# Performance work log

Measured on AMD Instinct MI355X. Metric: run time of the kernel, lower is better.

Reference implementation:

```python
import jax, jax.numpy as jnp
import numpy as np

NUM_EDGE_TYPES = 38
NUM_NODE_TYPES = 4
HIDDEN = 64
HOPS = 4
N_NODES = 100_000
N_EDGES = 1_600_000


def setup_inputs() -> dict:
    key = jax.random.key(0)
    ks = jax.random.split(key, 7)
    in_dim = NUM_EDGE_TYPES + 2 * NUM_NODE_TYPES  # 46
    return {
        "edge_index": jax.random.randint(ks[0], (2, N_EDGES), 0, N_NODES),
        "edge_type": jax.random.randint(ks[1], (N_EDGES,), 0, NUM_EDGE_TYPES),
        "node_type": jax.random.randint(ks[2], (N_NODES,), 0, NUM_NODE_TYPES),
        "W1": jax.random.normal(ks[3], (in_dim, HIDDEN), dtype=jnp.float32) * 0.1,
        "b1": jax.random.normal(ks[4], (HIDDEN,), dtype=jnp.float32) * 0.1,
        "W2": jax.random.normal(ks[5], (HIDDEN, 1), dtype=jnp.float32) * 0.1,
        "b2": jax.random.normal(ks[6], (1,), dtype=jnp.float32) * 0.1,
    }


def reference(edge_index, edge_type, node_type, W1, b1, W2, b2):
    src, dst = edge_index[0], edge_index[1]  # PyG: x_j = x[edge_index[0]], aggregate at edge_index[1]
    head_type = node_type[src]
    tail_type = node_type[dst]
    # Linear over concat of three one-hots == sum of three gathered weight rows + bias.
    h = (W1[edge_type]
         + W1[NUM_EDGE_TYPES + head_type]
         + W1[NUM_EDGE_TYPES + NUM_NODE_TYPES + tail_type]
         + b1)                                   # [E, HIDDEN]
    h = jax.nn.gelu(h)
    edge_emb = jax.nn.sigmoid(h @ W2 + b2)       # [E, 1]

    num_nodes = node_type.shape[0]
    aggr = jnp.zeros((num_nodes, 1), dtype=edge_emb.dtype)
    for _ in range(HOPS):
        msg = aggr[src] + edge_emb               # gather + add, [E, 1]
        aggr = jax.ops.segment_sum(msg, dst, num_segments=num_nodes)  # scatter-add
    return aggr
```

## Files before the change

### kernel.cpp

```cpp
#include <hip/hip_runtime.h>

#define NUM_EDGE_TYPES 38
#define NUM_NODE_TYPES 4
#define HIDDEN 64
#define TABLE_SIZE (NUM_EDGE_TYPES * NUM_NODE_TYPES * NUM_NODE_TYPES)
#define SRC_BITS 17
#define SRC_MASK ((1 << SRC_BITS) - 1)
#define BSHIFT 8
#define BNODES 256
#define MAXB 512
#define PB 512
#define EPT 16
#define CHUNK (PB * EPT)
#define HB 1024
#define CAPC 6144

__device__ __forceinline__ float table_entry(int i, const float* __restrict__ W1,
                                             const float* __restrict__ b1,
                                             const float* __restrict__ W2,
                                             const float* __restrict__ b2) {
    int et = i >> 4, ht = (i >> 2) & 3, tt = i & 3;
    const float* r0 = W1 + et * HIDDEN;
    const float* r1 = W1 + (NUM_EDGE_TYPES + ht) * HIDDEN;
    const float* r2 = W1 + (NUM_EDGE_TYPES + NUM_NODE_TYPES + tt) * HIDDEN;
    float acc = b2[0];
#pragma unroll 8
    for (int k = 0; k < HIDDEN; ++k) {
        float h = r0[k] + r1[k] + r2[k] + b1[k];
        float u = 0.7978845608028654f * (h + 0.044715f * h * h * h);
        float g = 0.5f * h * (1.0f + tanhf(u));
        acc += g * W2[k];
    }
    return 1.0f / (1.0f + expf(-acc));
}

__global__ void table_kernel(const float* __restrict__ W1, const float* __restrict__ b1,
                             const float* __restrict__ W2, const float* __restrict__ b2,
                             float* __restrict__ table) {
    int i = blockIdx.x * blockDim.x + threadIdx.x;
    if (i < TABLE_SIZE) table[i] = table_entry(i, W1, b1, W2, b2);
}

__global__ __launch_bounds__(PB)
void partition_kernel(const int* __restrict__ src, const int* __restrict__ dst,
                      const int* __restrict__ etype, int* __restrict__ cursor,
                      int* __restrict__ pack, int E, int nbk, int cap,
                      const float* __restrict__ W1, const float* __restrict__ b1,
                      const float* __restrict__ W2, const float* __restrict__ b2,
                      float* __restrict__ table) {
    __shared__ int hist[MAXB];
    __shared__ int locCur[MAXB];
    for (int i = threadIdx.x; i < nbk; i += PB) hist[i] = 0;
    __syncthreads();
    int start = blockIdx.x * CHUNK;
    int end = min(start + CHUNK, E);
    if (end - start == CHUNK) {
        int4 dv[4], sv[4], ev[4];
#pragma unroll
        for (int g = 0; g < 4; ++g) {
            int j = start + g * (PB * 4) + threadIdx.x * 4;
            dv[g] = *(const int4*)(dst + j);
        }
#pragma unroll
        for (int g = 0; g < 4; ++g) {
            atomicAdd(&hist[dv[g].x >> BSHIFT], 1);
            atomicAdd(&hist[dv[g].y >> BSHIFT], 1);
            atomicAdd(&hist[dv[g].z >> BSHIFT], 1);
            atomicAdd(&hist[dv[g].w >> BSHIFT], 1);
        }
#pragma unroll
        for (int g = 0; g < 4; ++g) {
            int j = start + g * (PB * 4) + threadIdx.x * 4;
            sv[g] = *(const int4*)(src + j);
            ev[g] = *(const int4*)(etype + j);
        }
        __syncthreads();
        for (int i = threadIdx.x; i < nbk; i += PB) {
            int h = hist[i];
            locCur[i] = h ? i * cap + atomicAdd(&cursor[i], h) : 0;
        }
        __syncthreads();
#pragma unroll
        for (int g = 0; g < 4; ++g) {
            int t0 = atomicAdd(&locCur[dv[g].x >> BSHIFT], 1);
            int t1 = atomicAdd(&locCur[dv[g].y >> BSHIFT], 1);
            int t2 = atomicAdd(&locCur[dv[g].z >> BSHIFT], 1);
            int t3 = atomicAdd(&locCur[dv[g].w >> BSHIFT], 1);
            pack[t0] = (ev[g].x << (SRC_BITS + 8)) | ((dv[g].x & (BNODES - 1)) << SRC_BITS) | sv[g].x;
            pack[t1] = (ev[g].y << (SRC_BITS + 8)) | ((dv[g].y & (BNODES - 1)) << SRC_BITS) | sv[g].y;
            pack[t2] = (ev[g].z << (SRC_BITS + 8)) | ((dv[g].z & (BNODES - 1)) << SRC_BITS) | sv[g].z;
            pack[t3] = (ev[g].w << (SRC_BITS + 8)) | ((dv[g].w & (BNODES - 1)) << SRC_BITS) | sv[g].w;
        }
    } else {
        for (int j = start + threadIdx.x; j < end; j += PB)
            atomicAdd(&hist[dst[j] >> BSHIFT], 1);
        __syncthreads();
        for (int i = threadIdx.x; i < nbk; i += PB) {
            int h = hist[i];
            locCur[i] = h ? i * cap + atomicAdd(&cursor[i], h) : 0;
        }
        __syncthreads();
        for (int j = start + threadIdx.x; j < end; j += PB) {
            int d = dst[j];
            int slot = atomicAdd(&locCur[d >> BSHIFT], 1);
            pack[slot] = (etype[j] << (SRC_BITS + 8)) | ((d & (BNODES - 1)) << SRC_BITS) | src[j];
        }
    }

    for (int seg = blockIdx.x; seg < 8; seg += gridDim.x) {
        int wid = threadIdx.x >> 6, lane = threadIdx.x & 63;
        int e0 = seg * 76;
        int e1 = min(e0 + 76, TABLE_SIZE);
        for (int e = e0 + wid; e < e1; e += PB / 64) {
            int et = e >> 4, ht = (e >> 2) & 3, tt = e & 3;
            float h = W1[et * HIDDEN + lane]
                    + W1[(NUM_EDGE_TYPES + ht) * HIDDEN + lane]
                    + W1[(NUM_EDGE_TYPES + NUM_NODE_TYPES + tt) * HIDDEN + lane]
                    + b1[lane];
            float u = 0.7978845608028654f * (h + 0.044715f * h * h * h);
            float g = 0.5f * h * (1.0f + tanhf(u));
            float v = g * W2[lane];
            v += __shfl_xor(v, 32, 64);
            v += __shfl_xor(v, 16, 64);
            v += __shfl_xor(v, 8, 64);
            v += __shfl_xor(v, 4, 64);
            v += __shfl_xor(v, 2, 64);
            v += __shfl_xor(v, 1, 64);
            if (lane == 0) table[e] = 1.0f / (1.0f + expf(-(v + b2[0])));
        }
    }
}

__global__ void sort_base_kernel(int* __restrict__ pack, const int* __restrict__ cursor,
                                 const int* __restrict__ ntype, const float* __restrict__ table,
                                 float* __restrict__ base, int* __restrict__ nodeOffG,
                                 int N, int cap) {
    __shared__ int rawL[CAPC];
    __shared__ int sortedL[CAPC];
    __shared__ float tbl[TABLE_SIZE];
    __shared__ int nodeCnt[BNODES];
    __shared__ int nodeOff[BNODES + 1];
    __shared__ unsigned char ntLoc[BNODES];
    int b = blockIdx.x;
    int node0 = b << BSHIFT;
    int tid = threadIdx.x;
    int st = b * cap;
    int c = min(cursor[b], cap);

    if (tid < TABLE_SIZE) tbl[tid] = table[tid];
    if (tid < BNODES) {
        nodeCnt[tid] = 0;
        int n = node0 + tid;
        ntLoc[tid] = (n < N) ? (unsigned char)ntype[n] : 0;
    }
    __syncthreads();

    int c4 = c & ~3;
    for (int j = tid * 4; j < c4; j += HB * 4) {
        int4 v = *(const int4*)(pack + st + j);
        *(int4*)(rawL + j) = v;
        atomicAdd(&nodeCnt[(v.x >> SRC_BITS) & (BNODES - 1)], 1);
        atomicAdd(&nodeCnt[(v.y >> SRC_BITS) & (BNODES - 1)], 1);
        atomicAdd(&nodeCnt[(v.z >> SRC_BITS) & (BNODES - 1)], 1);
        atomicAdd(&nodeCnt[(v.w >> SRC_BITS) & (BNODES - 1)], 1);
    }
    for (int j = c4 + tid; j < c; j += HB) {
        int p = pack[st + j];
        rawL[j] = p;
        atomicAdd(&nodeCnt[(p >> SRC_BITS) & (BNODES - 1)], 1);
    }
    __syncthreads();

    if (tid < 64) {
        int lane = tid;
        int v0 = nodeCnt[lane * 4], v1 = nodeCnt[lane * 4 + 1];
        int v2 = nodeCnt[lane * 4 + 2], v3 = nodeCnt[lane * 4 + 3];
        int s = v0 + v1 + v2 + v3;
        int inc = s;
        for (int d = 1; d < 64; d <<= 1) {
            int t = __shfl_up(inc, d, 64);
            if (lane >= d) inc += t;
        }
        int excl = inc - s;
        nodeOff[lane * 4]     = excl;
        nodeOff[lane * 4 + 1] = excl + v0;
        nodeOff[lane * 4 + 2] = excl + v0 + v1;
        nodeOff[lane * 4 + 3] = excl + v0 + v1 + v2;
        if (lane == 63) nodeOff[BNODES] = inc;
    }
    __syncthreads();
    if (tid < BNODES) nodeCnt[tid] = 0;
    __syncthreads();

    {
        int j = tid;
        for (; j + HB < c; j += 2 * HB) {
            int p0 = rawL[j];
            int p1 = rawL[j + HB];
            int dl0 = (p0 >> SRC_BITS) & (BNODES - 1);
            int dl1 = (p1 >> SRC_BITS) & (BNODES - 1);
            int r0 = atomicAdd(&nodeCnt[dl0], 1);
            int r1 = atomicAdd(&nodeCnt[dl1], 1);
            sortedL[nodeOff[dl0] + r0] = p0;
            sortedL[nodeOff[dl1] + r1] = p1;
        }
        if (j < c) {
            int p = rawL[j];
            int dl = (p >> SRC_BITS) & (BNODES - 1);
            int r = atomicAdd(&nodeCnt[dl], 1);
            sortedL[nodeOff[dl] + r] = p;
        }
    }
    __syncthreads();

    for (int j = tid * 4; j < c4; j += HB * 4)
        *(int4*)(pack + st + j) = *(const int4*)(sortedL + j);
    for (int j = c4 + tid; j < c; j += HB) pack[st + j] = sortedL[j];
    if (tid < BNODES) nodeOffG[(b << BSHIFT) + tid] = nodeOff[tid];

    int node = tid >> 2, l = tid & 3;
    int lo = nodeOff[node], hi = nodeOff[node + 1];
    int nt = ntLoc[node];
    float s = 0.0f;
    int j = lo + l;
    for (; j + 4 < hi; j += 8) {
        int p0 = sortedL[j], p1 = sortedL[j + 4];
        s += tbl[((((unsigned)p0) >> (SRC_BITS + 8)) << 4) | (ntype[p0 & SRC_MASK] << 2) | nt]
           + tbl[((((unsigned)p1) >> (SRC_BITS + 8)) << 4) | (ntype[p1 & SRC_MASK] << 2) | nt];
    }
    if (j < hi) {
        int p = sortedL[j];
        s += tbl[((((unsigned)p) >> (SRC_BITS + 8)) << 4) | (ntype[p & SRC_MASK] << 2) | nt];
    }
    s += __shfl_xor(s, 1, 64);
    s += __shfl_xor(s, 2, 64);
    int n = node0 + node;
    if (l == 0 && n < N) base[n] = s;
}

__global__ __launch_bounds__(512)
void hop_csr_kernel(const int* __restrict__ pack, const int* __restrict__ nodeOffG,
                    const int* __restrict__ cursor, const float* __restrict__ base,
                    const float* __restrict__ prev, float* __restrict__ out,
                    int N, int cap) {
    __shared__ int off[65];
    int blk = blockIdx.x;
    int b = blk >> 2;
    int q = blk & 3;
    int tid = threadIdx.x;
    int st = b * cap;
    int nodeBase = (b << BSHIFT) + q * 64;
    if (tid < 64) off[tid] = nodeOffG[nodeBase + tid];
    else if (tid == 64)
        off[64] = (q == 3) ? min(cursor[b], cap) : nodeOffG[nodeBase + 64];
    __syncthreads();
    int node = tid >> 3, l = tid & 7;
    int lo = off[node], hi = off[node + 1];
    float s = 0.0f;
    int j = st + lo + l;
    int hiG = st + hi;
    for (; j + 8 < hiG; j += 16) {
        int p0 = pack[j], p1 = pack[j + 8];
        s += prev[p0 & SRC_MASK] + prev[p1 & SRC_MASK];
    }
    if (j < hiG) s += prev[pack[j] & SRC_MASK];
    s += __shfl_xor(s, 1, 64);
    s += __shfl_xor(s, 2, 64);
    s += __shfl_xor(s, 4, 64);
    int n = nodeBase + node;
    if (l == 0 && n < N) out[n] = base[n] + s;
}

__global__ void edge_base_kernel(const int* __restrict__ src, const int* __restrict__ dst,
                                 const int* __restrict__ etype, const int* __restrict__ ntype,
                                 const float* __restrict__ table, float* __restrict__ base, int E) {
    __shared__ float tbl[TABLE_SIZE];
    for (int i = threadIdx.x; i < TABLE_SIZE; i += blockDim.x) tbl[i] = table[i];
    __syncthreads();
    int e = blockIdx.x * blockDim.x + threadIdx.x;
    if (e >= E) return;
    int s = src[e];
    int d = dst[e];
    int idx = (etype[e] << 4) | (ntype[s] << 2) | ntype[d];
    atomicAdd(base + d, tbl[idx]);
}

__global__ void copy_kernel(const float* __restrict__ in, float* __restrict__ out, int N) {
    int i = blockIdx.x * blockDim.x + threadIdx.x;
    if (i < N) out[i] = in[i];
}

__global__ void edge_hop_kernel(const int* __restrict__ src, const int* __restrict__ dst,
                                const float* __restrict__ prev, float* __restrict__ next, int E) {
    int e = blockIdx.x * blockDim.x + threadIdx.x;
    if (e >= E) return;
    atomicAdd(next + dst[e], prev[src[e]]);
}

extern "C" void kernel_launch(void* const* d_in, const int* in_sizes, int n_in,
                              void* d_out, int out_size, void* d_ws, size_t ws_size,
                              hipStream_t stream) {
    const int* edge_index = (const int*)d_in[0];
    const int* etype      = (const int*)d_in[1];
    const int* ntype      = (const int*)d_in[2];
    const float* W1       = (const float*)d_in[3];
    const float* b1       = (const float*)d_in[4];
    const float* W2       = (const float*)d_in[5];
    const float* b2       = (const float*)d_in[6];

    const int E = in_sizes[1];
    const int N = in_sizes[2];
    const int* src = edge_index;
    const int* dst = edge_index + E;
    float* out = (float*)d_out;

    const int nbk = (N + BNODES - 1) >> BSHIFT;
    const int nChunks = (E + CHUNK - 1) / CHUNK;

    int cap = ((E / (nbk > 0 ? nbk : 1)) * 3 / 2 + 255) & ~255;
    if (cap < 512) cap = 512;
    size_t packElems = (size_t)nbk * cap;

    size_t need = (packElems + MAXB + (size_t)nbk * BNODES + 1024 + (size_t)3 * N) * 4 + 256;

    if (ws_size >= need && nbk <= MAXB && cap <= CAPC) {
        int* pack     = (int*)d_ws;
        int* cursor   = pack + packElems;
        int* nodeOffG = cursor + MAXB;
        float* table  = (float*)(nodeOffG + (size_t)nbk * BNODES);
        float* base   = table + 1024;
        float* bufA   = base + N;
        float* bufB   = bufA + N;

        hipMemsetAsync(cursor, 0, MAXB * sizeof(int), stream);
        partition_kernel<<<nChunks, PB, 0, stream>>>(src, dst, etype, cursor, pack, E, nbk, cap,
                                                     W1, b1, W2, b2, table);
        sort_base_kernel<<<nbk, HB, 0, stream>>>(pack, cursor, ntype, table, base, nodeOffG, N, cap);
        hop_csr_kernel<<<4 * nbk, 512, 0, stream>>>(pack, nodeOffG, cursor, base, base, bufA, N, cap);
        hop_csr_kernel<<<4 * nbk, 512, 0, stream>>>(pack, nodeOffG, cursor, base, bufA, bufB, N, cap);
        hop_csr_kernel<<<4 * nbk, 512, 0, stream>>>(pack, nodeOffG, cursor, base, bufB, out, N, cap);
    } else {
        float* table = (float*)d_ws;
        float* base  = table + 1024;
        float* bufA  = base + N;
        float* bufB  = bufA + N;
        const int eb = (E + 255) / 256;
        const int nb = (N + 255) / 256;

        hipMemsetAsync(base, 0, (size_t)N * sizeof(float), stream);
        table_kernel<<<(TABLE_SIZE + 255) / 256, 256, 0, stream>>>(W1, b1, W2, b2, table);

        edge_base_kernel<<<eb, 256, 0, stream>>>(src, dst, etype, ntype, table, base, E);
        copy_kernel<<<nb, 256, 0, stream>>>(base, bufA, N);
        edge_hop_kernel<<<eb, 256, 0, stream>>>(src, dst, base, bufA, E);
        copy_kernel<<<nb, 256, 0, stream>>>(base, bufB, N);
        edge_hop_kernel<<<eb, 256, 0, stream>>>(src, dst, bufA, bufB, E);
        copy_kernel<<<nb, 256, 0, stream>>>(base, out, N);
        edge_hop_kernel<<<eb, 256, 0, stream>>>(src, dst, bufB, out, E);
    }
}
```

Baseline: 134.6 us.

## Shrink partition chunks, compact node types to bytes, widen hop lanes per node

The partition kernel now uses 1024-thread blocks that each handle 4 edges per thread, so there are many more, smaller chunks and more parallelism, at the cost of more global cursor atomics. It also writes a byte-sized copy of node_type, which sort_base reads for its random src-type lookups to cut gather traffic. The hop kernel assigns 16 lanes per node and 32 nodes per block with twice as many blocks, which shortens per-node serial loops but leaves more lanes idle on low-degree nodes.

Result: slower. 138.4 us (+2.8%).

```diff
diff --git a/kernel.cpp b/kernel.cpp
--- a/kernel.cpp
+++ b/kernel.cpp
@@ -9,8 +9,8 @@
 #define BSHIFT 8
 #define BNODES 256
 #define MAXB 512
-#define PB 512
-#define EPT 16
+#define PB 1024
+#define EPT 4
 #define CHUNK (PB * EPT)
 #define HB 1024
 #define CAPC 6144
@@ -44,10 +44,11 @@
 __global__ __launch_bounds__(PB)
 void partition_kernel(const int* __restrict__ src, const int* __restrict__ dst,
                       const int* __restrict__ etype, int* __restrict__ cursor,
-                      int* __restrict__ pack, int E, int nbk, int cap,
+                      int* __restrict__ pack, int E, int N, int nbk, int cap,
                       const float* __restrict__ W1, const float* __restrict__ b1,
                       const float* __restrict__ W2, const float* __restrict__ b2,
-                      float* __restrict__ table) {
+                      float* __restrict__ table, const int* __restrict__ ntype,
+                      unsigned char* __restrict__ ntu8) {
     __shared__ int hist[MAXB];
     __shared__ int locCur[MAXB];
     for (int i = threadIdx.x; i < nbk; i += PB) hist[i] = 0;
@@ -55,42 +56,28 @@
     int start = blockIdx.x * CHUNK;
     int end = min(start + CHUNK, E);
     if (end - start == CHUNK) {
-        int4 dv[4], sv[4], ev[4];
-#pragma unroll
-        for (int g = 0; g < 4; ++g) {
-            int j = start + g * (PB * 4) + threadIdx.x * 4;
-            dv[g] = *(const int4*)(dst + j);
-        }
-#pragma unroll
-        for (int g = 0; g < 4; ++g) {
-            atomicAdd(&hist[dv[g].x >> BSHIFT], 1);
-            atomicAdd(&hist[dv[g].y >> BSHIFT], 1);
-            atomicAdd(&hist[dv[g].z >> BSHIFT], 1);
-            atomicAdd(&hist[dv[g].w >> BSHIFT], 1);
-        }
-#pragma unroll
-        for (int g = 0; g < 4; ++g) {
-            int j = start + g * (PB * 4) + threadIdx.x * 4;
-            sv[g] = *(const int4*)(src + j);
-            ev[g] = *(const int4*)(etype + j);
-        }
+        int j = start + threadIdx.x * 4;
+        int4 dv = *(const int4*)(dst + j);
+        atomicAdd(&hist[dv.x >> BSHIFT], 1);
+        atomicAdd(&hist[dv.y >> BSHIFT], 1);
+        atomicAdd(&hist[dv.z >> BSHIFT], 1);
+        atomicAdd(&hist[dv.w >> BSHIFT], 1);
+        int4 sv = *(const int4*)(src + j);
+        int4 ev = *(const int4*)(etype + j);
         __syncthreads();
         for (int i = threadIdx.x; i < nbk; i += PB) {
             int h = hist[i];
             locCur[i] = h ? i * cap + atomicAdd(&cursor[i], h) : 0;
         }
         __syncthreads();
-#pragma unroll
-        for (int g = 0; g < 4; ++g) {
-            int t0 = atomicAdd(&locCur[dv[g].x >> BSHIFT], 1);
-            int t1 = atomicAdd(&locCur[dv[g].y >> BSHIFT], 1);
-            int t2 = atomicAdd(&locCur[dv[g].z >> BSHIFT], 1);
-            int t3 = atomicAdd(&locCur[dv[g].w >> BSHIFT], 1);
-            pack[t0] = (ev[g].x << (SRC_BITS + 8)) | ((dv[g].x & (BNODES - 1)) << SRC_BITS) | sv[g].x;
-            pack[t1] = (ev[g].y << (SRC_BITS + 8)) | ((dv[g].y & (BNODES - 1)) << SRC_BITS) | sv[g].y;
-            pack[t2] = (ev[g].z << (SRC_BITS + 8)) | ((dv[g].z & (BNODES - 1)) << SRC_BITS) | sv[g].z;
-            pack[t3] = (ev[g].w << (SRC_BITS + 8)) | ((dv[g].w & (BNODES - 1)) << SRC_BITS) | sv[g].w;
-        }
+        int t0 = atomicAdd(&locCur[dv.x >> BSHIFT], 1);
+        int t1 = atomicAdd(&locCur[dv.y >> BSHIFT], 1);
+        int t2 = atomicAdd(&locCur[dv.z >> BSHIFT], 1);
+        int t3 = atomicAdd(&locCur[dv.w >> BSHIFT], 1);
+        pack[t0] = (ev.x << (SRC_BITS + 8)) | ((dv.x & (BNODES - 1)) << SRC_BITS) | sv.x;
+        pack[t1] = (ev.y << (SRC_BITS + 8)) | ((dv.y & (BNODES - 1)) << SRC_BITS) | sv.y;
+        pack[t2] = (ev.z << (SRC_BITS + 8)) | ((dv.z & (BNODES - 1)) << SRC_BITS) | sv.z;
+        pack[t3] = (ev.w << (SRC_BITS + 8)) | ((dv.w & (BNODES - 1)) << SRC_BITS) | sv.w;
     } else {
         for (int j = start + threadIdx.x; j < end; j += PB)
             atomicAdd(&hist[dst[j] >> BSHIFT], 1);
@@ -106,6 +93,9 @@
             pack[slot] = (etype[j] << (SRC_BITS + 8)) | ((d & (BNODES - 1)) << SRC_BITS) | src[j];
         }
     }
+
+    for (int i = blockIdx.x * PB + threadIdx.x; i < N; i += gridDim.x * PB)
+        ntu8[i] = (unsigned char)ntype[i];
 
     for (int seg = blockIdx.x; seg < 8; seg += gridDim.x) {
         int wid = threadIdx.x >> 6, lane = threadIdx.x & 63;
@@ -132,7 +122,8 @@
 }
 
 __global__ void sort_base_kernel(int* __restrict__ pack, const int* __restrict__ cursor,
-                                 const int* __restrict__ ntype, const float* __restrict__ table,
+                                 const unsigned char* __restrict__ ntu8,
+                                 const float* __restrict__ table,
                                  float* __restrict__ base, int* __restrict__ nodeOffG,
                                  int N, int cap) {
     __shared__ int rawL[CAPC];
@@ -151,7 +142,7 @@
     if (tid < BNODES) {
         nodeCnt[tid] = 0;
         int n = node0 + tid;
-        ntLoc[tid] = (n < N) ? (unsigned char)ntype[n] : 0;
+        ntLoc[tid] = (n < N) ? ntu8[n] : (unsigned char)0;
     }
     __syncthreads();
 
@@ -225,12 +216,12 @@
     int j = lo + l;
     for (; j + 4 < hi; j += 8) {
         int p0 = sortedL[j], p1 = sortedL[j + 4];
-        s += tbl[((((unsigned)p0) >> (SRC_BITS + 8)) << 4) | (ntype[p0 & SRC_MASK] << 2) | nt]
-           + tbl[((((unsigned)p1) >> (SRC_BITS + 8)) << 4) | (ntype[p1 & SRC_MASK] << 2) | nt];
+        s += tbl[((((unsigned)p0) >> (SRC_BITS + 8)) << 4) | ((int)ntu8[p0 & SRC_MASK] << 2) | nt]
+           + tbl[((((unsigned)p1) >> (SRC_BITS + 8)) << 4) | ((int)ntu8[p1 & SRC_MASK] << 2) | nt];
     }
     if (j < hi) {
         int p = sortedL[j];
-        s += tbl[((((unsigned)p) >> (SRC_BITS + 8)) << 4) | (ntype[p & SRC_MASK] << 2) | nt];
+        s += tbl[((((unsigned)p) >> (SRC_BITS + 8)) << 4) | ((int)ntu8[p & SRC_MASK] << 2) | nt];
     }
     s += __shfl_xor(s, 1, 64);
     s += __shfl_xor(s, 2, 64);
@@ -243,30 +234,27 @@
                     const int* __restrict__ cursor, const float* __restrict__ base,
                     const float* __restrict__ prev, float* __restrict__ out,
                     int N, int cap) {
-    __shared__ int off[65];
+    __shared__ int off[33];
     int blk = blockIdx.x;
-    int b = blk >> 2;
-    int q = blk & 3;
+    int b = blk >> 3;
+    int q = blk & 7;
     int tid = threadIdx.x;
     int st = b * cap;
-    int nodeBase = (b << BSHIFT) + q * 64;
-    if (tid < 64) off[tid] = nodeOffG[nodeBase + tid];
-    else if (tid == 64)
-        off[64] = (q == 3) ? min(cursor[b], cap) : nodeOffG[nodeBase + 64];
-    __syncthreads();
-    int node = tid >> 3, l = tid & 7;
+    int nodeBase = (b << BSHIFT) + q * 32;
+    if (tid < 32) off[tid] = nodeOffG[nodeBase + tid];
+    else if (tid == 32)
+        off[32] = (q == 7) ? min(cursor[b], cap) : nodeOffG[nodeBase + 32];
+    __syncthreads();
+    int node = tid >> 4, l = tid & 15;
     int lo = off[node], hi = off[node + 1];
     float s = 0.0f;
-    int j = st + lo + l;
     int hiG = st + hi;
-    for (; j + 8 < hiG; j += 16) {
-        int p0 = pack[j], p1 = pack[j + 8];
-        s += prev[p0 & SRC_MASK] + prev[p1 & SRC_MASK];
-    }
-    if (j < hiG) s += prev[pack[j] & SRC_MASK];
+    for (int j = st + lo + l; j < hiG; j += 16)
+        s += prev[pack[j] & SRC_MASK];
     s += __shfl_xor(s, 1, 64);
     s += __shfl_xor(s, 2, 64);
     s += __shfl_xor(s, 4, 64);
+    s += __shfl_xor(s, 8, 64);
     int n = nodeBase + node;
     if (l == 0 && n < N) out[n] = base[n] + s;
 }
@@ -321,7 +309,8 @@
     if (cap < 512) cap = 512;
     size_t packElems = (size_t)nbk * cap;
 
-    size_t need = (packElems + MAXB + (size_t)nbk * BNODES + 1024 + (size_t)3 * N) * 4 + 256;
+    size_t need = (packElems + MAXB + (size_t)nbk * BNODES + 1024 + (size_t)3 * N
+                   + ((size_t)N + 3) / 4) * 4 + 256;
 
     if (ws_size >= need && nbk <= MAXB && cap <= CAPC) {
         int* pack     = (int*)d_ws;
@@ -331,14 +320,15 @@
         float* base   = table + 1024;
         float* bufA   = base + N;
         float* bufB   = bufA + N;
+        unsigned char* ntu8 = (unsigned char*)(bufB + N);
 
         hipMemsetAsync(cursor, 0, MAXB * sizeof(int), stream);
-        partition_kernel<<<nChunks, PB, 0, stream>>>(src, dst, etype, cursor, pack, E, nbk, cap,
-                                                     W1, b1, W2, b2, table);
-        sort_base_kernel<<<nbk, HB, 0, stream>>>(pack, cursor, ntype, table, base, nodeOffG, N, cap);
-        hop_csr_kernel<<<4 * nbk, 512, 0, stream>>>(pack, nodeOffG, cursor, base, base, bufA, N, cap);
-        hop_csr_kernel<<<4 * nbk, 512, 0, stream>>>(pack, nodeOffG, cursor, base, bufA, bufB, N, cap);
-        hop_csr_kernel<<<4 * nbk, 512, 0, stream>>>(pack, nodeOffG, cursor, base, bufB, out, N, cap);
+        partition_kernel<<<nChunks, PB, 0, stream>>>(src, dst, etype, cursor, pack, E, N, nbk, cap,
+                                                     W1, b1, W2, b2, table, ntype, ntu8);
+        sort_base_kernel<<<nbk, HB, 0, stream>>>(pack, cursor, ntu8, table, base, nodeOffG, N, cap);
+        hop_csr_kernel<<<8 * nbk, 512, 0, stream>>>(pack, nodeOffG, cursor, base, base, bufA, N, cap);
+        hop_csr_kernel<<<8 * nbk, 512, 0, stream>>>(pack, nodeOffG, cursor, base, bufA, bufB, N, cap);
+        hop_csr_kernel<<<8 * nbk, 512, 0, stream>>>(pack, nodeOffG, cursor, base, bufB, out, N, cap);
     } else {
         float* table = (float*)d_ws;
         float* base  = table + 1024;
```

## Stage partitioned edges in LDS by bucket before coalesced global writes

Applied to the files above, without the earlier changes.

The partition kernel now prefix-sums the per-block bucket histogram, scatters packed edge words into a shared-memory staging buffer grouped by destination bucket, and then writes them to global memory in contiguous runs. A binary search over bucket offsets finds each slot's destination. This is meant to replace fully random global scatter writes with mostly contiguous ones. Edges per thread are halved to fit the 16KB stage buffer, which doubles the block count and the number of global cursor atomics. It also adds extra synchronization and the per-element binary search.

New measurement: 137.8 us. 2.3% more time.

```diff
diff --git a/kernel.cpp b/kernel.cpp
--- a/kernel.cpp
+++ b/kernel.cpp
@@ -10,7 +10,7 @@
 #define BNODES 256
 #define MAXB 512
 #define PB 512
-#define EPT 16
+#define EPT 8
 #define CHUNK (PB * EPT)
 #define HB 1024
 #define CAPC 6144
@@ -49,60 +49,87 @@
                       const float* __restrict__ W2, const float* __restrict__ b2,
                       float* __restrict__ table) {
     __shared__ int hist[MAXB];
-    __shared__ int locCur[MAXB];
-    for (int i = threadIdx.x; i < nbk; i += PB) hist[i] = 0;
+    __shared__ int bkOff[MAXB + 1];
+    __shared__ int locS[MAXB];
+    __shared__ int stage[CHUNK];
+    int tid = threadIdx.x;
+    for (int i = tid; i < MAXB; i += PB) hist[i] = 0;
     __syncthreads();
     int start = blockIdx.x * CHUNK;
     int end = min(start + CHUNK, E);
     if (end - start == CHUNK) {
-        int4 dv[4], sv[4], ev[4];
-#pragma unroll
-        for (int g = 0; g < 4; ++g) {
-            int j = start + g * (PB * 4) + threadIdx.x * 4;
+        int4 dv[2], sv[2], ev[2];
+#pragma unroll
+        for (int g = 0; g < 2; ++g) {
+            int j = start + g * (PB * 4) + tid * 4;
             dv[g] = *(const int4*)(dst + j);
-        }
-#pragma unroll
-        for (int g = 0; g < 4; ++g) {
+            sv[g] = *(const int4*)(src + j);
+            ev[g] = *(const int4*)(etype + j);
+        }
+#pragma unroll
+        for (int g = 0; g < 2; ++g) {
             atomicAdd(&hist[dv[g].x >> BSHIFT], 1);
             atomicAdd(&hist[dv[g].y >> BSHIFT], 1);
             atomicAdd(&hist[dv[g].z >> BSHIFT], 1);
             atomicAdd(&hist[dv[g].w >> BSHIFT], 1);
         }
-#pragma unroll
-        for (int g = 0; g < 4; ++g) {
-            int j = start + g * (PB * 4) + threadIdx.x * 4;
-            sv[g] = *(const int4*)(src + j);
-            ev[g] = *(const int4*)(etype + j);
-        }
-        __syncthreads();
-        for (int i = threadIdx.x; i < nbk; i += PB) {
+        __syncthreads();
+        if (tid < 64) {
+            int bi = tid * 8;
+            int v[8]; int s = 0;
+#pragma unroll
+            for (int k = 0; k < 8; ++k) { v[k] = hist[bi + k]; s += v[k]; }
+            int inc = s;
+            for (int d = 1; d < 64; d <<= 1) {
+                int t = __shfl_up(inc, d, 64);
+                if (tid >= d) inc += t;
+            }
+            int excl = inc - s;
+#pragma unroll
+            for (int k = 0; k < 8; ++k) { bkOff[bi + k] = excl; excl += v[k]; }
+            if (tid == 63) bkOff[MAXB] = inc;
+        }
+        for (int i = tid; i < nbk; i += PB) {
             int h = hist[i];
-            locCur[i] = h ? i * cap + atomicAdd(&cursor[i], h) : 0;
-        }
-        __syncthreads();
-#pragma unroll
-        for (int g = 0; g < 4; ++g) {
-            int t0 = atomicAdd(&locCur[dv[g].x >> BSHIFT], 1);
-            int t1 = atomicAdd(&locCur[dv[g].y >> BSHIFT], 1);
-            int t2 = atomicAdd(&locCur[dv[g].z >> BSHIFT], 1);
-            int t3 = atomicAdd(&locCur[dv[g].w >> BSHIFT], 1);
-            pack[t0] = (ev[g].x << (SRC_BITS + 8)) | ((dv[g].x & (BNODES - 1)) << SRC_BITS) | sv[g].x;
-            pack[t1] = (ev[g].y << (SRC_BITS + 8)) | ((dv[g].y & (BNODES - 1)) << SRC_BITS) | sv[g].y;
-            pack[t2] = (ev[g].z << (SRC_BITS + 8)) | ((dv[g].z & (BNODES - 1)) << SRC_BITS) | sv[g].z;
-            pack[t3] = (ev[g].w << (SRC_BITS + 8)) | ((dv[g].w & (BNODES - 1)) << SRC_BITS) | sv[g].w;
+            locS[i] = h ? i * cap + atomicAdd(&cursor[i], h) : 0;
+        }
+        __syncthreads();
+        for (int i = tid; i < MAXB; i += PB) hist[i] = 0;
+        __syncthreads();
+#pragma unroll
+        for (int g = 0; g < 2; ++g) {
+            int w0 = (ev[g].x << (SRC_BITS + 8)) | ((dv[g].x & (BNODES - 1)) << SRC_BITS) | sv[g].x;
+            int w1 = (ev[g].y << (SRC_BITS + 8)) | ((dv[g].y & (BNODES - 1)) << SRC_BITS) | sv[g].y;
+            int w2 = (ev[g].z << (SRC_BITS + 8)) | ((dv[g].z & (BNODES - 1)) << SRC_BITS) | sv[g].z;
+            int w3 = (ev[g].w << (SRC_BITS + 8)) | ((dv[g].w & (BNODES - 1)) << SRC_BITS) | sv[g].w;
+            int b0 = dv[g].x >> BSHIFT, b1_ = dv[g].y >> BSHIFT;
+            int b2_ = dv[g].z >> BSHIFT, b3 = dv[g].w >> BSHIFT;
+            stage[bkOff[b0] + atomicAdd(&hist[b0], 1)] = w0;
+            stage[bkOff[b1_] + atomicAdd(&hist[b1_], 1)] = w1;
+            stage[bkOff[b2_] + atomicAdd(&hist[b2_], 1)] = w2;
+            stage[bkOff[b3] + atomicAdd(&hist[b3], 1)] = w3;
+        }
+        __syncthreads();
+        for (int j = tid; j < CHUNK; j += PB) {
+            int lo = 0, hi = MAXB;
+            while (hi - lo > 1) {
+                int mid = (lo + hi) >> 1;
+                if (bkOff[mid] <= j) lo = mid; else hi = mid;
+            }
+            pack[locS[lo] + (j - bkOff[lo])] = stage[j];
         }
     } else {
-        for (int j = start + threadIdx.x; j < end; j += PB)
+        for (int j = start + tid; j < end; j += PB)
             atomicAdd(&hist[dst[j] >> BSHIFT], 1);
         __syncthreads();
-        for (int i = threadIdx.x; i < nbk; i += PB) {
+        for (int i = tid; i < nbk; i += PB) {
             int h = hist[i];
-            locCur[i] = h ? i * cap + atomicAdd(&cursor[i], h) : 0;
-        }
-        __syncthreads();
-        for (int j = start + threadIdx.x; j < end; j += PB) {
+            locS[i] = h ? i * cap + atomicAdd(&cursor[i], h) : 0;
+        }
+        __syncthreads();
+        for (int j = start + tid; j < end; j += PB) {
             int d = dst[j];
-            int slot = atomicAdd(&locCur[d >> BSHIFT], 1);
+            int slot = atomicAdd(&locS[d >> BSHIFT], 1);
             pack[slot] = (etype[j] << (SRC_BITS + 8)) | ((d & (BNODES - 1)) << SRC_BITS) | src[j];
         }
     }
```
